# Optimization experiments

Measured on AMD Instinct MI355X. Metric: run time of the kernel, lower is better.

Reference implementation:

```python
import jax, jax.numpy as jnp
import numpy as np

VOC_SIZE = 512
CHAR_EMB = 128
N_FILT = 16
KERNELS = [2, 3, 4, 5, 6]
PADS = [0, 0, 1, 2, 3]
B, L = 16384, 32


def _conv1d(x, w, b, pad):
    # x: [B, C, L], w: [O, I, K] -> [B, O, L_out]
    y = jax.lax.conv_general_dilated(
        x, w, window_strides=(1,), padding=[(pad, pad)],
        dimension_numbers=("NCH", "OIH", "NCH"))
    return y + b[None, :, None]


def setup_inputs() -> dict:
    key = jax.random.key(0)
    ks = jax.random.split(key, 12)
    word = jax.random.randint(ks[0], (B, L), 0, VOC_SIZE, dtype=jnp.int64 if jax.config.jax_enable_x64 else jnp.int32)
    emb = jax.random.normal(ks[1], (VOC_SIZE, CHAR_EMB), dtype=jnp.float32) * 0.1
    inp = {"word": word, "emb": emb}
    for i, k in enumerate(KERNELS):
        fan_in = CHAR_EMB * k
        bound = 1.0 / np.sqrt(fan_in)
        inp[f"w{k}"] = jax.random.uniform(ks[2 + 2 * i], (N_FILT, CHAR_EMB, k), jnp.float32, -bound, bound)
        inp[f"b{k}"] = jax.random.uniform(ks[3 + 2 * i], (N_FILT,), jnp.float32, -bound, bound)
    return inp


def reference(word, emb, w2, b2, w3, b3, w4, b4, w5, b5, w6, b6):
    unk = word < 0                      # [B, L]
    idx = jnp.where(unk, 0, word)
    x = emb[idx]                        # [B, L, E]
    x = jnp.where(unk[..., None], 0.0, x)
    x = jnp.transpose(x, (0, 2, 1))     # [B, E, L]
    ws = [w2, w3, w4, w5, w6]
    bs = [b2, b3, b4, b5, b6]
    maxima = [jnp.max(_conv1d(x, w, b, p), axis=-1)
              for w, b, p in zip(ws, bs, PADS)]  # each [B, 16]
    return jnp.concatenate(maxima, axis=-1)      # [B, 80]
```

## Files before the change

### kernel.cpp

```cpp
#include <hip/hip_runtime.h>
#include <hip/hip_fp16.h>

#define VOC      512
#define EMB      128
#define L_SEQ    32
#define NWORDS   16384
#define NCOL     416
#define WPB      128
#define SCP      48

__device__ __constant__ int SUBBASE[10] = {0, 8208, 16416, 32832, 49248,
                                           65664, 82080, 114912, 147744, 180576};
__device__ __constant__ int SUBW[10]    = {16, 16, 32, 32, 32, 32, 64, 64, 64, 64};

__global__ __launch_bounds__(512) void build_pe(
    const float* __restrict__ emb,
    const float* __restrict__ w2, const float* __restrict__ w3,
    const float* __restrict__ w4, const float* __restrict__ w5,
    const float* __restrict__ w6,
    __half* __restrict__ pe)
{
    __shared__ float e[4][EMB];
    const int tid = threadIdx.x;
    const int c0  = blockIdx.x * 4;
    {
        const int ch = tid >> 7, i = tid & 127;
        const int c  = c0 + ch;
        e[ch][i] = (c < VOC) ? emb[c * EMB + i] : 0.f;
    }
    __syncthreads();

    const int col = tid;
    if (col >= NCOL) return;

    int k, jpad, base, seg; const float* w;
    if (col < 32)       { k = 2; jpad = 2; base = 0;   seg = 0; w = w2; }
    else if (col < 96)  { k = 3; jpad = 4; base = 32;  seg = 1; w = w3; }
    else if (col < 160) { k = 4; jpad = 4; base = 96;  seg = 2; w = w4; }
    else if (col < 288) { k = 5; jpad = 8; base = 160; seg = 3; w = w5; }
    else                { k = 6; jpad = 8; base = 288; seg = 4; w = w6; }

    const int r   = col - base;
    const int ol  = (jpad == 2) ? (r >> 1) : (jpad == 4) ? (r >> 2) : (r >> 3);
    const int j   = r & (jpad - 1);
    const int sub = seg * 2 + (ol >> 3);
    const int loc = (ol & 7) * jpad + j;

    float a0 = 0.f, a1 = 0.f, a2 = 0.f, a3 = 0.f;
    if (j < k) {
        const float* wp = w + (ol * EMB) * k + j;
        #pragma unroll 8
        for (int i = 0; i < EMB; ++i) {
            const float wv = wp[i * k];
            a0 += wv * e[0][i]; a1 += wv * e[1][i];
            a2 += wv * e[2][i]; a3 += wv * e[3][i];
        }
    }
    const int W = SUBW[sub], Bb = SUBBASE[sub];
    const float a[4] = {a0, a1, a2, a3};
    #pragma unroll
    for (int ch = 0; ch < 4; ++ch) {
        const int c = c0 + ch;
        if (c <= VOC) pe[Bb + c * W + loc] = __float2half(a[ch]);
    }
}

__device__ __forceinline__ float2 h2tof2(int u) {
    return __half22float2(__builtin_bit_cast(__half2, u));
}

template<int K> struct LdT;
template<> struct LdT<2> { using T = int;  };
template<> struct LdT<3> { using T = int2; };
template<> struct LdT<4> { using T = int2; };
template<> struct LdT<5> { using T = int4; };
template<> struct LdT<6> { using T = int4; };

template<int K>
__device__ __forceinline__ void unpack(typename LdT<K>::T q, float* v) {
    if constexpr (K == 2) {
        float2 f = h2tof2(q); v[0] = f.x; v[1] = f.y;
    } else if constexpr (K == 3) {
        float2 f0 = h2tof2(q.x), f1 = h2tof2(q.y);
        v[0] = f0.x; v[1] = f0.y; v[2] = f1.x;
    } else if constexpr (K == 4) {
        float2 f0 = h2tof2(q.x), f1 = h2tof2(q.y);
        v[0] = f0.x; v[1] = f0.y; v[2] = f1.x; v[3] = f1.y;
    } else if constexpr (K == 5) {
        float2 f0 = h2tof2(q.x), f1 = h2tof2(q.y), f2 = h2tof2(q.z);
        v[0] = f0.x; v[1] = f0.y; v[2] = f1.x; v[3] = f1.y; v[4] = f2.x;
    } else {
        float2 f0 = h2tof2(q.x), f1 = h2tof2(q.y), f2 = h2tof2(q.z);
        v[0] = f0.x; v[1] = f0.y; v[2] = f1.x; v[3] = f1.y;
        v[4] = f2.x; v[5] = f2.y;
    }
}

template<int K, int PAD, int LANEB>
__device__ __forceinline__ float convseg(
    const char* __restrict__ tb, const unsigned short* __restrict__ sc,
    int w, int lb, float bias)
{
    using LT = typename LdT<K>::T;
    constexpr int LOUT = L_SEQ + 2 * PAD - K + 1;

    int4 s4[4];
    {
        const int4* sp = (const int4*)(sc + w * SCP);
        #pragma unroll
        for (int g = 0; g < 4; ++g) s4[g] = sp[g];
    }

    float s[LOUT];
    #pragma unroll
    for (int t = 0; t < LOUT; ++t) s[t] = bias;

    #pragma unroll
    for (int g = 0; g < 4; ++g) {
        const int dd[4] = {s4[g].x, s4[g].y, s4[g].z, s4[g].w};
        LT q[8];
        #pragma unroll
        for (int u = 0; u < 8; ++u) {
            const int pm = (u & 1) ? (int)(((unsigned)dd[u >> 1]) >> 16)
                                   : (dd[u >> 1] & 0xffff);
            q[u] = *(const LT*)(tb + (pm << 1) + lb);
        }
        #pragma unroll
        for (int u = 0; u < 8; ++u) {
            const int tp = g * 8 + u;
            float v[K];
            unpack<K>(q[u], v);
            #pragma unroll
            for (int j = 0; j < K; ++j) {
                const int t = tp + PAD - j;
                if (t >= 0 && t < LOUT) s[t] += v[j];
            }
        }
    }

    float m = s[0];
    #pragma unroll
    for (int t = 1; t < LOUT; ++t) m = fmaxf(m, s[t]);
    return m;
}

__global__ __launch_bounds__(512, 4) void conv_max(
    const int*    __restrict__ word,
    const __half* __restrict__ pe,
    const float* __restrict__ b2, const float* __restrict__ b3,
    const float* __restrict__ b4, const float* __restrict__ b5,
    const float* __restrict__ b6,
    float*       __restrict__ out)
{
    __shared__ __align__(16) __half tab[513 * 64];
    __shared__ __align__(16) unsigned short sc16[WPB * SCP];

    const int tid  = threadIdx.x;
    const int sub  = blockIdx.x % 10;
    const int wb   = blockIdx.x / 10;
    const int seg  = sub >> 1;
    const int half = sub & 1;

    const int  W16 = SUBW[sub];
    const int  nI4 = (513 * W16) >> 3;
    const int4* src = (const int4*)(pe + SUBBASE[sub]);
    int4* dst = (int4*)tab;
    for (int i = tid; i < nI4; i += 512) dst[i] = src[i];

    const int shb = (seg == 0) ? 4 : (seg <= 2) ? 5 : 6;
    #pragma unroll
    for (int r = 0; r < 8; ++r) {
        const int i  = tid + r * 512;
        const int c  = word[wb * (WPB * L_SEQ) + i];
        const int ce = (c >= 0) ? c : VOC;
        sc16[(i >> 5) * SCP + (i & 31)] = (unsigned short)(ce << shb);
    }
    __syncthreads();

    const int ol = tid & 7;
    const int w0 = tid >> 3;
    const float* bp = (seg == 0) ? b2 : (seg == 1) ? b3 :
                      (seg == 2) ? b4 : (seg == 3) ? b5 : b6;
    const float bias = bp[half * 8 + ol];
    const char* tb = (const char*)tab;

    float m0, m1;
    switch (seg) {
        case 0:  m0 = convseg<2, 0, 4 >(tb, sc16, w0,      ol * 4,  bias);
                 m1 = convseg<2, 0, 4 >(tb, sc16, w0 + 64, ol * 4,  bias); break;
        case 1:  m0 = convseg<3, 0, 8 >(tb, sc16, w0,      ol * 8,  bias);
                 m1 = convseg<3, 0, 8 >(tb, sc16, w0 + 64, ol * 8,  bias); break;
        case 2:  m0 = convseg<4, 1, 8 >(tb, sc16, w0,      ol * 8,  bias);
                 m1 = convseg<4, 1, 8 >(tb, sc16, w0 + 64, ol * 8,  bias); break;
        case 3:  m0 = convseg<5, 2, 16>(tb, sc16, w0,      ol * 16, bias);
                 m1 = convseg<5, 2, 16>(tb, sc16, w0 + 64, ol * 16, bias); break;
        default: m0 = convseg<6, 3, 16>(tb, sc16, w0,      ol * 16, bias);
                 m1 = convseg<6, 3, 16>(tb, sc16, w0 + 64, ol * 16, bias); break;
    }
    const int oc = seg * 16 + half * 8 + ol;
    out[(wb * WPB + w0     ) * 80 + oc] = m0;
    out[(wb * WPB + w0 + 64) * 80 + oc] = m1;
}

extern "C" void kernel_launch(void* const* d_in, const int* in_sizes, int n_in,
                              void* d_out, int out_size, void* d_ws, size_t ws_size,
                              hipStream_t stream)
{
    const int*   word = (const int*)  d_in[0];
    const float* emb  = (const float*)d_in[1];
    const float* w2   = (const float*)d_in[2];
    const float* b2   = (const float*)d_in[3];
    const float* w3   = (const float*)d_in[4];
    const float* b3   = (const float*)d_in[5];
    const float* w4   = (const float*)d_in[6];
    const float* b4   = (const float*)d_in[7];
    const float* w5   = (const float*)d_in[8];
    const float* b5   = (const float*)d_in[9];
    const float* w6   = (const float*)d_in[10];
    const float* b6   = (const float*)d_in[11];
    float* out = (float*)d_out;

    __half* pe16 = (__half*)d_ws;

    build_pe<<<129, 512, 0, stream>>>(emb, w2, w3, w4, w5, w6, pe16);

    conv_max<<<10 * (NWORDS / WPB), 512, 0, stream>>>(
        word, pe16, b2, b3, b4, b5, b6, out);
}
```

Baseline: 103.6 us.

## Repartition conv work into 13 uniform sub-tables with ring-buffer streaming max

Result: slower. 151.9 us (+46.6%).

```diff
diff --git a/kernel.cpp b/kernel.cpp
--- a/kernel.cpp
+++ b/kernel.cpp
@@ -1,17 +1,17 @@
 #include <hip/hip_runtime.h>
 #include <hip/hip_fp16.h>
 
-#define VOC      512
-#define EMB      128
-#define L_SEQ    32
-#define NWORDS   16384
-#define NCOL     416
-#define WPB      128
-#define SCP      48
-
-__device__ __constant__ int SUBBASE[10] = {0, 8208, 16416, 32832, 49248,
-                                           65664, 82080, 114912, 147744, 180576};
-__device__ __constant__ int SUBW[10]    = {16, 16, 32, 32, 32, 32, 64, 64, 64, 64};
+#define VOC    512
+#define EMB    128
+#define L_SEQ  32
+#define NWORDS 16384
+#define NCOL   416
+#define WPB    128
+#define NSUB   13
+#define SUBH   32
+#define ROWH   40
+#define SCP    40
+
 
 __global__ __launch_bounds__(512) void build_pe(
     const float* __restrict__ emb,
@@ -20,16 +20,14 @@
     const float* __restrict__ w6,
     __half* __restrict__ pe)
 {
-    __shared__ float e[4][EMB];
+    __shared__ float e[2][EMB];
     const int tid = threadIdx.x;
-    const int c0  = blockIdx.x * 4;
-    {
-        const int ch = tid >> 7, i = tid & 127;
-        const int c  = c0 + ch;
+    const int c0  = blockIdx.x * 2;
+    if (tid < 2 * EMB) {
+        const int ch = tid >> 7, i = tid & 127, c = c0 + ch;
         e[ch][i] = (c < VOC) ? emb[c * EMB + i] : 0.f;
     }
     __syncthreads();
-
     const int col = tid;
     if (col >= NCOL) return;
 
@@ -40,111 +38,110 @@
     else if (col < 288) { k = 5; jpad = 8; base = 160; seg = 3; w = w5; }
     else                { k = 6; jpad = 8; base = 288; seg = 4; w = w6; }
 
-    const int r   = col - base;
-    const int ol  = (jpad == 2) ? (r >> 1) : (jpad == 4) ? (r >> 2) : (r >> 3);
-    const int j   = r & (jpad - 1);
-    const int sub = seg * 2 + (ol >> 3);
-    const int loc = (ol & 7) * jpad + j;
-
-    float a0 = 0.f, a1 = 0.f, a2 = 0.f, a3 = 0.f;
+    const int r  = col - base;
+    const int ol = (jpad == 2) ? (r >> 1) : (jpad == 4) ? (r >> 2) : (r >> 3);
+    const int j  = r & (jpad - 1);
+
+    int sub, loc;
+    if (seg == 0)      { sub = 0;           loc = ol * 2 + j; }
+    else if (seg == 1) { sub = 1 + (ol>>3); loc = (ol & 7) * 4 + j; }
+    else if (seg == 2) { sub = 3 + (ol>>3); loc = (ol & 7) * 4 + j; }
+    else if (seg == 3) { sub = 5 + (ol>>2); loc = (ol & 3) * 8 + j; }
+    else               { sub = 9 + (ol>>2); loc = (ol & 3) * 8 + j; }
+
+    float a0 = 0.f, a1 = 0.f;
     if (j < k) {
         const float* wp = w + (ol * EMB) * k + j;
         #pragma unroll 8
         for (int i = 0; i < EMB; ++i) {
             const float wv = wp[i * k];
             a0 += wv * e[0][i]; a1 += wv * e[1][i];
-            a2 += wv * e[2][i]; a3 += wv * e[3][i];
-        }
-    }
-    const int W = SUBW[sub], Bb = SUBBASE[sub];
-    const float a[4] = {a0, a1, a2, a3};
-    #pragma unroll
-    for (int ch = 0; ch < 4; ++ch) {
-        const int c = c0 + ch;
-        if (c <= VOC) pe[Bb + c * W + loc] = __float2half(a[ch]);
-    }
+        }
+    }
+    const int bb = sub * (513 * SUBH) + loc;
+    pe[bb + c0 * SUBH] = __float2half(a0);
+    if (c0 + 1 <= VOC) pe[bb + (c0 + 1) * SUBH] = __float2half(a1);
 }
 
 __device__ __forceinline__ float2 h2tof2(int u) {
     return __half22float2(__builtin_bit_cast(__half2, u));
 }
 
-template<int K> struct LdT;
-template<> struct LdT<2> { using T = int;  };
-template<> struct LdT<3> { using T = int2; };
-template<> struct LdT<4> { using T = int2; };
-template<> struct LdT<5> { using T = int4; };
-template<> struct LdT<6> { using T = int4; };
-
-template<int K>
-__device__ __forceinline__ void unpack(typename LdT<K>::T q, float* v) {
-    if constexpr (K == 2) {
-        float2 f = h2tof2(q); v[0] = f.x; v[1] = f.y;
-    } else if constexpr (K == 3) {
-        float2 f0 = h2tof2(q.x), f1 = h2tof2(q.y);
-        v[0] = f0.x; v[1] = f0.y; v[2] = f1.x;
-    } else if constexpr (K == 4) {
-        float2 f0 = h2tof2(q.x), f1 = h2tof2(q.y);
-        v[0] = f0.x; v[1] = f0.y; v[2] = f1.x; v[3] = f1.y;
-    } else if constexpr (K == 5) {
-        float2 f0 = h2tof2(q.x), f1 = h2tof2(q.y), f2 = h2tof2(q.z);
-        v[0] = f0.x; v[1] = f0.y; v[2] = f1.x; v[3] = f1.y; v[4] = f2.x;
-    } else {
-        float2 f0 = h2tof2(q.x), f1 = h2tof2(q.y), f2 = h2tof2(q.z);
-        v[0] = f0.x; v[1] = f0.y; v[2] = f1.x; v[3] = f1.y;
-        v[4] = f2.x; v[5] = f2.y;
-    }
-}
-
-template<int K, int PAD, int LANEB>
-__device__ __forceinline__ float convseg(
-    const char* __restrict__ tb, const unsigned short* __restrict__ sc,
-    int w, int lb, float bias)
-{
-    using LT = typename LdT<K>::T;
+template<int K, int PAD, int NF, int JP>
+__device__ __forceinline__ void convseg(
+    const char* __restrict__ tbl,
+    const unsigned short* __restrict__ sc,
+    int w, float* __restrict__ mm)
+{
     constexpr int LOUT = L_SEQ + 2 * PAD - K + 1;
 
-    int4 s4[4];
+    int d[16];
     {
         const int4* sp = (const int4*)(sc + w * SCP);
         #pragma unroll
-        for (int g = 0; g < 4; ++g) s4[g] = sp[g];
-    }
-
-    float s[LOUT];
+        for (int g = 0; g < 4; ++g) {
+            const int4 s = sp[g];
+            d[4*g] = s.x; d[4*g+1] = s.y; d[4*g+2] = s.z; d[4*g+3] = s.w;
+        }
+    }
+
+    float ring[NF][K];
+    float mx[NF];
     #pragma unroll
-    for (int t = 0; t < LOUT; ++t) s[t] = bias;
+    for (int f = 0; f < NF; ++f) mx[f] = -3.0e38f;
 
     #pragma unroll
-    for (int g = 0; g < 4; ++g) {
-        const int dd[4] = {s4[g].x, s4[g].y, s4[g].z, s4[g].w};
-        LT q[8];
-        #pragma unroll
-        for (int u = 0; u < 8; ++u) {
-            const int pm = (u & 1) ? (int)(((unsigned)dd[u >> 1]) >> 16)
-                                   : (dd[u >> 1] & 0xffff);
-            q[u] = *(const LT*)(tb + (pm << 1) + lb);
-        }
-        #pragma unroll
-        for (int u = 0; u < 8; ++u) {
-            const int tp = g * 8 + u;
-            float v[K];
-            unpack<K>(q[u], v);
+    for (int tp = 0; tp < 32; ++tp) {
+        const int dw = d[tp >> 1];
+        const int pm = (tp & 1) ? (int)(((unsigned)dw) >> 16) : (dw & 0xffff);
+        float v[NF][JP];
+        if constexpr (JP == 2) {
+            const int2 qq = *(const int2*)(tbl + pm);
+            const float2 f0 = h2tof2(qq.x), f1 = h2tof2(qq.y);
+            v[0][0]=f0.x; v[0][1]=f0.y; v[1][0]=f1.x; v[1][1]=f1.y;
+        } else if constexpr (NF == 2) {
+            const int4 qq = *(const int4*)(tbl + pm);
+            const float2 a0=h2tof2(qq.x), a1=h2tof2(qq.y);
+            const float2 c0=h2tof2(qq.z), c1=h2tof2(qq.w);
+            v[0][0]=a0.x; v[0][1]=a0.y; v[0][2]=a1.x; v[0][3]=a1.y;
+            v[1][0]=c0.x; v[1][1]=c0.y; v[1][2]=c1.x; v[1][3]=c1.y;
+        } else {
+            const int4 qq = *(const int4*)(tbl + pm);
+            const float2 a0=h2tof2(qq.x), a1=h2tof2(qq.y), a2=h2tof2(qq.z);
+            v[0][0]=a0.x; v[0][1]=a0.y; v[0][2]=a1.x; v[0][3]=a1.y;
+            v[0][4]=a2.x;
+            if constexpr (K >= 6) v[0][5]=a2.y;
+        }
+        #pragma unroll
+        for (int j = 0; j < K; ++j) {
+            const int t = tp + PAD - j;
+            if (t < 0 || t >= LOUT) continue;
+            const bool first = (tp == ((t >= PAD) ? (t - PAD) : 0));
             #pragma unroll
-            for (int j = 0; j < K; ++j) {
-                const int t = tp + PAD - j;
-                if (t >= 0 && t < LOUT) s[t] += v[j];
+            for (int f = 0; f < NF; ++f) {
+                if (first) ring[f][t % K]  = v[f][j];
+                else       ring[f][t % K] += v[f][j];
             }
         }
-    }
-
-    float m = s[0];
+        const int tr = tp + PAD - (K - 1);
+        if (tr >= 0 && tr < LOUT) {
+            #pragma unroll
+            for (int f = 0; f < NF; ++f)
+                mx[f] = fmaxf(mx[f], ring[f][tr % K]);
+        }
+    }
+    constexpr int TT = (32 + PAD - K + 1 > 0) ? (32 + PAD - K + 1) : 0;
     #pragma unroll
-    for (int t = 1; t < LOUT; ++t) m = fmaxf(m, s[t]);
-    return m;
-}
-
-__global__ __launch_bounds__(512, 4) void conv_max(
+    for (int t = TT; t < LOUT; ++t)
+        #pragma unroll
+        for (int f = 0; f < NF; ++f)
+            mx[f] = fmaxf(mx[f], ring[f][t % K]);
+
+    mm[0] = mx[0];
+    if constexpr (NF == 2) mm[1] = mx[1];
+}
+
+__global__ __launch_bounds__(512, 6) void conv_max(
     const int*    __restrict__ word,
     const __half* __restrict__ pe,
     const float* __restrict__ b2, const float* __restrict__ b3,
@@ -152,54 +149,73 @@
     const float* __restrict__ b6,
     float*       __restrict__ out)
 {
-    __shared__ __align__(16) __half tab[513 * 64];
+    __shared__ __align__(16) __half tab[513 * ROWH];
     __shared__ __align__(16) unsigned short sc16[WPB * SCP];
 
-    const int tid  = threadIdx.x;
-    const int sub  = blockIdx.x % 10;
-    const int wb   = blockIdx.x / 10;
-    const int seg  = sub >> 1;
-    const int half = sub & 1;
-
-    const int  W16 = SUBW[sub];
-    const int  nI4 = (513 * W16) >> 3;
-    const int4* src = (const int4*)(pe + SUBBASE[sub]);
-    int4* dst = (int4*)tab;
-    for (int i = tid; i < nI4; i += 512) dst[i] = src[i];
-
-    const int shb = (seg == 0) ? 4 : (seg <= 2) ? 5 : 6;
-    #pragma unroll
-    for (int r = 0; r < 8; ++r) {
-        const int i  = tid + r * 512;
-        const int c  = word[wb * (WPB * L_SEQ) + i];
-        const int ce = (c >= 0) ? c : VOC;
-        sc16[(i >> 5) * SCP + (i & 31)] = (unsigned short)(ce << shb);
+    const int tid = threadIdx.x;
+    const int sub = blockIdx.x % NSUB;
+    const int wb  = blockIdx.x / NSUB;
+
+    {
+        const int4* src = (const int4*)(pe + sub * (513 * SUBH));
+        char* tw = (char*)tab;
+        for (int i = tid; i < 513 * 4; i += 512)
+            *(int4*)(tw + (i >> 2) * 80 + (i & 3) * 16) = src[i];
+    }
+    {
+        const int base = wb * (WPB * L_SEQ);
+        #pragma unroll
+        for (int r = 0; r < 8; ++r) {
+            const int i = tid + r * 512;
+            const int c = word[base + i];
+            const int ce = (c >= 0) ? c : VOC;
+            sc16[(i >> 5) * SCP + (i & 31)] = (unsigned short)(ce * 80);
+        }
     }
     __syncthreads();
 
-    const int ol = tid & 7;
-    const int w0 = tid >> 3;
-    const float* bp = (seg == 0) ? b2 : (seg == 1) ? b3 :
-                      (seg == 2) ? b4 : (seg == 3) ? b5 : b6;
-    const float bias = bp[half * 8 + ol];
-    const char* tb = (const char*)tab;
-
-    float m0, m1;
-    switch (seg) {
-        case 0:  m0 = convseg<2, 0, 4 >(tb, sc16, w0,      ol * 4,  bias);
-                 m1 = convseg<2, 0, 4 >(tb, sc16, w0 + 64, ol * 4,  bias); break;
-        case 1:  m0 = convseg<3, 0, 8 >(tb, sc16, w0,      ol * 8,  bias);
-                 m1 = convseg<3, 0, 8 >(tb, sc16, w0 + 64, ol * 8,  bias); break;
-        case 2:  m0 = convseg<4, 1, 8 >(tb, sc16, w0,      ol * 8,  bias);
-                 m1 = convseg<4, 1, 8 >(tb, sc16, w0 + 64, ol * 8,  bias); break;
-        case 3:  m0 = convseg<5, 2, 16>(tb, sc16, w0,      ol * 16, bias);
-                 m1 = convseg<5, 2, 16>(tb, sc16, w0 + 64, ol * 16, bias); break;
-        default: m0 = convseg<6, 3, 16>(tb, sc16, w0,      ol * 16, bias);
-                 m1 = convseg<6, 3, 16>(tb, sc16, w0 + 64, ol * 16, bias); break;
-    }
-    const int oc = seg * 16 + half * 8 + ol;
-    out[(wb * WPB + w0     ) * 80 + oc] = m0;
-    out[(wb * WPB + w0 + 64) * 80 + oc] = m1;
+    const char* tb    = (const char*)tab;
+    const int   wbase = wb * WPB;
+
+    int seg, q;
+    if (sub == 0)     { seg = 0; q = 0; }
+    else if (sub < 3) { seg = 1; q = sub - 1; }
+    else if (sub < 5) { seg = 2; q = sub - 3; }
+    else if (sub < 9) { seg = 3; q = sub - 5; }
+    else              { seg = 4; q = sub - 9; }
+
+    if (seg == 0) {
+        const int fp = tid & 7, w0 = tid >> 3;
+        const char* tbl = tb + fp * 8;
+        float m0[2], m1[2];
+        convseg<2, 0, 2, 2>(tbl, sc16, w0,      m0);
+        convseg<2, 0, 2, 2>(tbl, sc16, w0 + 64, m1);
+        const float bb0 = b2[2*fp], bb1 = b2[2*fp + 1];
+        float* o0 = out + (wbase + w0     ) * 80;
+        float* o1 = out + (wbase + w0 + 64) * 80;
+        o0[2*fp] = bb0 + m0[0]; o0[2*fp+1] = bb1 + m0[1];
+        o1[2*fp] = bb0 + m1[0]; o1[2*fp+1] = bb1 + m1[1];
+    } else if (seg <= 2) {
+        const int fp = tid & 3, w0 = tid >> 2;
+        const char* tbl = tb + fp * 16;
+        float m[2];
+        if (seg == 1) convseg<3, 0, 2, 4>(tbl, sc16, w0, m);
+        else          convseg<4, 1, 2, 4>(tbl, sc16, w0, m);
+        const float* bp = (seg == 1) ? b3 : b4;
+        const int f0 = q * 8 + 2 * fp;
+        float* o = out + (wbase + w0) * 80 + seg * 16;
+        o[f0]     = bp[f0]     + m[0];
+        o[f0 + 1] = bp[f0 + 1] + m[1];
+    } else {
+        const int ol = tid & 3, w0 = tid >> 2;
+        const char* tbl = tb + ol * 16;
+        float m[1];
+        if (seg == 3) convseg<5, 2, 1, 8>(tbl, sc16, w0, m);
+        else          convseg<6, 3, 1, 8>(tbl, sc16, w0, m);
+        const float* bp = (seg == 3) ? b5 : b6;
+        const int f = q * 4 + ol;
+        out[(wbase + w0) * 80 + seg * 16 + f] = bp[f] + m[0];
+    }
 }
 
 extern "C" void kernel_launch(void* const* d_in, const int* in_sizes, int n_in,
@@ -222,8 +238,8 @@
 
     __half* pe16 = (__half*)d_ws;
 
-    build_pe<<<129, 512, 0, stream>>>(emb, w2, w3, w4, w5, w6, pe16);
-
-    conv_max<<<10 * (NWORDS / WPB), 512, 0, stream>>>(
+    build_pe<<<257, 512, 0, stream>>>(emb, w2, w3, w4, w5, w6, pe16);
+
+    conv_max<<<NSUB * (NWORDS / WPB), 512, 0, stream>>>(
         word, pe16, b2, b3, b4, b5, b6, out);
 }
```
